# Kernel optimization log

Measured on AMD Instinct MI355X. Metric: run time of the kernel, lower is better.

The kernel has to match this reference:

```python
import jax, jax.numpy as jnp
import numpy as np
import math

B, L, D, H = 32, 512, 4096, 32
HD = D // H  # head_dim = 128


def setup_inputs() -> dict:
    key = jax.random.key(0)
    ks = jax.random.split(key, 9)
    s = 1.0 / math.sqrt(D)
    return {
        "x": jax.random.normal(ks[0], (B, L, D), jnp.float32),
        "Wq": jax.random.normal(ks[1], (D, D), jnp.float32) * s,
        "bq": jax.random.normal(ks[2], (D,), jnp.float32) * s,
        "Wk": jax.random.normal(ks[3], (D, D), jnp.float32) * s,
        "bk": jax.random.normal(ks[4], (D,), jnp.float32) * s,
        "Wv": jax.random.normal(ks[5], (D, D), jnp.float32) * s,
        "bv": jax.random.normal(ks[6], (D,), jnp.float32) * s,
        "Wo": jax.random.normal(ks[7], (D, D), jnp.float32) * s,
        "bo": jax.random.normal(ks[8], (D,), jnp.float32) * s,
    }


def reference(x, Wq, bq, Wk, bk, Wv, bv, Wo, bo):
    b, l, d = x.shape
    h, hd = H, HD
    # torch Linear: y = x @ W.T + b
    q = (x @ Wq.T + bq).reshape(b, l, h, hd).transpose(0, 2, 1, 3)  # [b,h,l,hd]
    k = (x @ Wk.T + bk).reshape(b, l, h, hd).transpose(0, 2, 1, 3)
    v = (x @ Wv.T + bv).reshape(b, l, h, hd).transpose(0, 2, 1, 3)
    scores = jnp.einsum("bhqd,bhkd->bhqk", q, k) / math.sqrt(hd)  # [b,h,L,L]
    # causal mask (upper triangle, diagonal=1, excluded)
    causal = jnp.tril(jnp.ones((l, l), bool))
    scores = jnp.where(causal, scores, -jnp.inf)
    att = jax.nn.softmax(scores, axis=-1)
    out = jnp.einsum("bhqk,bhkd->bhqd", att, v)  # [b,h,L,hd]
    out = out.transpose(0, 2, 1, 3).reshape(b, l, d)
    return out @ Wo.T + bo
```

## Files before the change

kernel.cpp:

```cpp
#include <hip/hip_runtime.h>
#include <cstdint>
#include <cstddef>

typedef __bf16 bf16_t;
typedef __bf16 bf16x8 __attribute__((ext_vector_type(8)));
typedef float f32x4 __attribute__((ext_vector_type(4)));

#define LOG2E 1.4426950408889634f

__device__ __forceinline__ void async16(const void* g, void* l) {
  __builtin_amdgcn_global_load_lds(
      (__attribute__((address_space(1))) unsigned int*)g,
      (__attribute__((address_space(3))) unsigned int*)l, 16, 0, 0);
}

__global__ void mha_cast_bf16(const float* __restrict__ s, bf16_t* __restrict__ d) {
  size_t i = (size_t)blockIdx.x * 256 + threadIdx.x;
  const float4* s4 = (const float4*)s;
  float4 a = s4[2 * i], b = s4[2 * i + 1];
  union { bf16_t h[8]; uint4 v; } u;
  u.h[0] = (bf16_t)a.x; u.h[1] = (bf16_t)a.y; u.h[2] = (bf16_t)a.z; u.h[3] = (bf16_t)a.w;
  u.h[4] = (bf16_t)b.x; u.h[5] = (bf16_t)b.y; u.h[6] = (bf16_t)b.z; u.h[7] = (bf16_t)b.w;
  ((uint4*)d)[i] = u.v;
}

__global__ void mha_cast_cat3(const float* __restrict__ s0, const float* __restrict__ s1,
                              const float* __restrict__ s2, bf16_t* __restrict__ d) {
  size_t i = (size_t)blockIdx.x * 256 + threadIdx.x;
  size_t e = i * 8;
  int r = (int)(e >> 24);
  const float* s = (r == 0) ? s0 : ((r == 1) ? s1 : s2);
  size_t off = e & 0xFFFFFFull;
  const float4* s4 = (const float4*)(s + off);
  float4 a = s4[0], b = s4[1];
  union { bf16_t h[8]; uint4 v; } u;
  u.h[0] = (bf16_t)a.x; u.h[1] = (bf16_t)a.y; u.h[2] = (bf16_t)a.z; u.h[3] = (bf16_t)a.w;
  u.h[4] = (bf16_t)b.x; u.h[5] = (bf16_t)b.y; u.h[6] = (bf16_t)b.z; u.h[7] = (bf16_t)b.w;
  ((uint4*)d)[i] = u.v;
}

template <int OUTF32>
__global__ __launch_bounds__(256, 2) void mha_gemm_bt(
    const bf16_t* __restrict__ A, const bf16_t* __restrict__ B,
    const float* __restrict__ b0, const float* __restrict__ b1,
    const float* __restrict__ b2, void* __restrict__ Cp,
    int N, int K, int tilesN) {
  __shared__ bf16_t As[128 * 32];
  __shared__ bf16_t Bs[128 * 32];
  const int tid = threadIdx.x;
  const int lane = tid & 63, w = tid >> 6;
  const int quad = lane >> 4, l16 = lane & 15;
  const int bm = blockIdx.x / tilesN, bn = blockIdx.x % tilesN;
  const int row0 = bm * 128, col0 = bn * 128;
  const int wm = (w >> 1) * 64, wn = (w & 1) * 64;

  f32x4 acc[4][4] = {};

  const int c0 = tid, c1 = 256 + tid;
  const int k80 = c0 >> 7, m0 = c0 & 127;
  const int k81 = c1 >> 7, m1 = c1 & 127;
  const bf16_t* gA0 = A + (size_t)(row0 + m0) * K + k80 * 8;
  const bf16_t* gA1 = A + (size_t)(row0 + m1) * K + k81 * 8;
  const bf16_t* gB0 = B + (size_t)(col0 + m0) * K + k80 * 8;
  const bf16_t* gB1 = B + (size_t)(col0 + m1) * K + k81 * 8;
  bf16_t* lA0 = As + (w * 64) * 8;
  bf16_t* lA1 = As + (256 + w * 64) * 8;
  bf16_t* lB0 = Bs + (w * 64) * 8;
  bf16_t* lB1 = Bs + (256 + w * 64) * 8;

  for (int k0 = 0; k0 < K; k0 += 32) {
    async16(gA0, lA0); async16(gA1, lA1);
    async16(gB0, lB0); async16(gB1, lB1);
    gA0 += 32; gA1 += 32; gB0 += 32; gB1 += 32;
    __syncthreads();
    bf16x8 af[4], bfr[4];
#pragma unroll
    for (int t = 0; t < 4; ++t)
      af[t] = *(const bf16x8*)(As + (quad * 128 + wm + 16 * t + l16) * 8);
#pragma unroll
    for (int u = 0; u < 4; ++u)
      bfr[u] = *(const bf16x8*)(Bs + (quad * 128 + wn + 16 * u + l16) * 8);
#pragma unroll
    for (int t = 0; t < 4; ++t)
#pragma unroll
      for (int u = 0; u < 4; ++u)
        acc[t][u] = __builtin_amdgcn_mfma_f32_16x16x32_bf16(af[t], bfr[u], acc[t][u], 0, 0, 0);
    __syncthreads();
  }

#pragma unroll
  for (int u = 0; u < 4; ++u) {
    int col = col0 + wn + 16 * u + l16;
    int sel = col >> 12;
    const float* bb = (sel == 0) ? b0 : ((sel == 1) ? b1 : b2);
    float bias = bb[col & 4095];
#pragma unroll
    for (int t = 0; t < 4; ++t) {
#pragma unroll
      for (int r = 0; r < 4; ++r) {
        int row = row0 + wm + 16 * t + quad * 4 + r;
        float val = acc[t][u][r] + bias;
        if (OUTF32)
          ((float*)Cp)[(size_t)row * N + col] = val;
        else
          ((bf16_t*)Cp)[(size_t)row * N + col] = (bf16_t)val;
      }
    }
  }
}

__global__ __launch_bounds__(256, 2) void mha_attn(const bf16_t* __restrict__ qkv,
                                                   bf16_t* __restrict__ out) {
  __shared__ bf16_t Ks[64 * 128];
  __shared__ bf16_t R2[128 * 128];
  const int tid = threadIdx.x;
  const int lane = tid & 63, w = tid >> 6;
  const int quad = lane >> 4, l16 = lane & 15;
  const int qt = blockIdx.x & 3;
  const int h = (blockIdx.x >> 2) & 31;
  const int b = blockIdx.x >> 7;
  const float scale = 0.08838834764831845f;
  const size_t rs = 12288;

  const bf16_t* baseQ = qkv + (size_t)(b * 512 + qt * 128) * rs + h * 128;
#pragma unroll
  for (int i = 0; i < 8; ++i) {
    int c = i * 256 + tid;
    int hd8 = c >> 7, m = c & 127;
    async16(baseQ + (size_t)m * rs + hd8 * 8, R2 + (i * 256 + w * 64) * 8);
  }
  __syncthreads();
  bf16x8 qf[2][4];
#pragma unroll
  for (int t = 0; t < 2; ++t)
#pragma unroll
    for (int kk = 0; kk < 4; ++kk)
      qf[t][kk] = *(const bf16x8*)(R2 + ((kk * 4 + quad) * 128 + w * 32 + 16 * t + l16) * 8);

  f32x4 O[2][8] = {};
  float mrow[2][4], lrow[2][4];
#pragma unroll
  for (int t = 0; t < 2; ++t)
#pragma unroll
    for (int r = 0; r < 4; ++r) { mrow[t][r] = -1e30f; lrow[t][r] = 0.f; }

  bf16_t* Vts = R2;
  bf16_t* Ps = R2 + 8192 + w * 2048;

  const int ktEnd = 2 * qt + 1;
  for (int kt = 0; kt <= ktEnd; ++kt) {
    __syncthreads();
    const bf16_t* baseK = qkv + (size_t)(b * 512 + kt * 64) * rs + 4096 + h * 128;
#pragma unroll
    for (int i = 0; i < 4; ++i) {
      int c = i * 256 + tid;
      int hd8 = c >> 6, key = c & 63;
      async16(baseK + (size_t)key * rs + hd8 * 8, Ks + (i * 256 + w * 64) * 8);
    }
    const bf16_t* baseV = qkv + (size_t)(b * 512 + kt * 64) * rs + 8192 + h * 128;
#pragma unroll
    for (int j = 0; j < 4; ++j) {
      int idx = j * 256 + tid;
      int d8 = idx & 15, key = idx >> 4;
      bf16x8 vv = *(const bf16x8*)(baseV + (size_t)key * rs + d8 * 8);
#pragma unroll
      for (int e = 0; e < 8; ++e) {
        int ee = (e + d8) & 7;
        int d = d8 * 8 + ee;
        Vts[((key >> 3) * 128 + d) * 8 + (key & 7)] = vv[ee];
      }
    }
    __syncthreads();

    f32x4 S[2][4] = {};
#pragma unroll
    for (int kk = 0; kk < 4; ++kk) {
      bf16x8 kf[4];
#pragma unroll
      for (int u = 0; u < 4; ++u)
        kf[u] = *(const bf16x8*)(Ks + ((kk * 4 + quad) * 64 + 16 * u + l16) * 8);
#pragma unroll
      for (int t = 0; t < 2; ++t)
#pragma unroll
        for (int u = 0; u < 4; ++u)
          S[t][u] = __builtin_amdgcn_mfma_f32_16x16x32_bf16(qf[t][kk], kf[u], S[t][u], 0, 0, 0);
    }

    const bool maskTile = (kt >= 2 * qt);
#pragma unroll
    for (int t = 0; t < 2; ++t) {
      int qbase = qt * 128 + w * 32 + 16 * t + quad * 4;
#pragma unroll
      for (int u = 0; u < 4; ++u) {
        int key = kt * 64 + 16 * u + l16;
#pragma unroll
        for (int r = 0; r < 4; ++r) {
          float v = S[t][u][r] * scale;
          if (maskTile && key > qbase + r) v = -1e30f;
          S[t][u][r] = v;
        }
      }
    }

#pragma unroll
    for (int t = 0; t < 2; ++t) {
#pragma unroll
      for (int r = 0; r < 4; ++r) {
        float mx = fmaxf(fmaxf(S[t][0][r], S[t][1][r]), fmaxf(S[t][2][r], S[t][3][r]));
        mx = fmaxf(mx, __shfl_xor(mx, 1));
        mx = fmaxf(mx, __shfl_xor(mx, 2));
        mx = fmaxf(mx, __shfl_xor(mx, 4));
        mx = fmaxf(mx, __shfl_xor(mx, 8));
        float mnew = fmaxf(mrow[t][r], mx);
        float alpha = exp2f((mrow[t][r] - mnew) * LOG2E);
        mrow[t][r] = mnew;
        float psum = 0.f;
#pragma unroll
        for (int u = 0; u < 4; ++u) {
          float p = exp2f((S[t][u][r] - mnew) * LOG2E);
          S[t][u][r] = p;
          psum += p;
        }
        psum += __shfl_xor(psum, 1);
        psum += __shfl_xor(psum, 2);
        psum += __shfl_xor(psum, 4);
        psum += __shfl_xor(psum, 8);
        lrow[t][r] = lrow[t][r] * alpha + psum;
#pragma unroll
        for (int u = 0; u < 8; ++u) O[t][u][r] *= alpha;
      }
    }

#pragma unroll
    for (int t = 0; t < 2; ++t)
#pragma unroll
      for (int u = 0; u < 4; ++u) {
        int key = 16 * u + l16;
#pragma unroll
        for (int rr = 0; rr < 4; ++rr) {
          int r = (rr + quad) & 3;
          Ps[((key >> 3) * 32 + 16 * t + quad * 4 + r) * 8 + (key & 7)] = (bf16_t)S[t][u][r];
        }
      }

#pragma unroll
    for (int kk = 0; kk < 2; ++kk) {
      bf16x8 pf[2], vf[8];
#pragma unroll
      for (int t = 0; t < 2; ++t)
        pf[t] = *(const bf16x8*)(Ps + ((kk * 4 + quad) * 32 + 16 * t + l16) * 8);
#pragma unroll
      for (int u = 0; u < 8; ++u)
        vf[u] = *(const bf16x8*)(Vts + ((kk * 4 + quad) * 128 + 16 * u + l16) * 8);
#pragma unroll
      for (int t = 0; t < 2; ++t)
#pragma unroll
        for (int u = 0; u < 8; ++u)
          O[t][u] = __builtin_amdgcn_mfma_f32_16x16x32_bf16(pf[t], vf[u], O[t][u], 0, 0, 0);
    }
  }

  bf16_t* outBase = out + (size_t)(b * 512 + qt * 128) * 4096 + h * 128;
#pragma unroll
  for (int t = 0; t < 2; ++t)
#pragma unroll
    for (int u = 0; u < 8; ++u) {
      int d = 16 * u + l16;
#pragma unroll
      for (int r = 0; r < 4; ++r) {
        int q = w * 32 + 16 * t + quad * 4 + r;
        float val = O[t][u][r] / lrow[t][r];
        outBase[(size_t)q * 4096 + d] = (bf16_t)val;
      }
    }
}

extern "C" void kernel_launch(void* const* d_in, const int* in_sizes, int n_in,
                              void* d_out, int out_size, void* d_ws, size_t ws_size,
                              hipStream_t stream) {
  const float* x  = (const float*)d_in[0];
  const float* Wq = (const float*)d_in[1];
  const float* bq = (const float*)d_in[2];
  const float* Wk = (const float*)d_in[3];
  const float* bk = (const float*)d_in[4];
  const float* Wv = (const float*)d_in[5];
  const float* bv = (const float*)d_in[6];
  const float* Wo = (const float*)d_in[7];
  const float* bo = (const float*)d_in[8];

  char* ws = (char*)d_ws;
  bf16_t* xb   = (bf16_t*)ws;
  bf16_t* wqkv = (bf16_t*)(ws + 134217728ull);
  bf16_t* wob  = (bf16_t*)(ws + 134217728ull + 100663296ull);
  bf16_t* qkvb = (bf16_t*)(ws + 134217728ull + 100663296ull + 33554432ull);

  mha_cast_bf16<<<32768, 256, 0, stream>>>(x, xb);
  mha_cast_cat3<<<24576, 256, 0, stream>>>(Wq, Wk, Wv, wqkv);
  mha_cast_bf16<<<8192, 256, 0, stream>>>(Wo, wob);

  mha_gemm_bt<0><<<12288, 256, 0, stream>>>(xb, wqkv, bq, bk, bv, qkvb, 12288, 4096, 96);

  mha_attn<<<4096, 256, 0, stream>>>(qkvb, xb);

  mha_gemm_bt<1><<<4096, 256, 0, stream>>>(xb, wob, bo, bo, bo, d_out, 4096, 4096, 32);
}
```

Baseline: 5.897 ms.

## Rewrite GEMM with 256x256 tiles, double-buffered async LDS and grid swizzle

Replaces the 128x128, single-buffered GEMM with a 512-thread 256x256 tile that double-buffers K=64 slices in 128KB of LDS using async global-to-LDS loads. Loads for the next-but-one tile are issued between the two MFMA halves, so memory traffic overlaps compute and the per-iteration sync shrinks to a waitcnt plus barrier. A blockIdx swizzle groups workgroups to improve L2 reuse. The cost is higher register pressure (128 accumulator floats per thread) and large LDS use, which limits occupancy to about one workgroup per CU.

```diff
diff --git a/kernel.cpp b/kernel.cpp
--- a/kernel.cpp
+++ b/kernel.cpp
@@ -39,67 +39,107 @@
   ((uint4*)d)[i] = u.v;
 }
 
+__device__ __forceinline__ void stage8(const bf16_t* ga, const bf16_t* gb,
+                                       bf16_t* la, bf16_t* lb) {
+  async16(ga,      la);
+  async16(ga + 16, la + 4096);
+  async16(ga + 32, la + 8192);
+  async16(ga + 48, la + 12288);
+  async16(gb,      lb);
+  async16(gb + 16, lb + 4096);
+  async16(gb + 32, lb + 8192);
+  async16(gb + 48, lb + 12288);
+}
+
 template <int OUTF32>
-__global__ __launch_bounds__(256, 2) void mha_gemm_bt(
+__global__ __launch_bounds__(512, 2) void mha_gemm_bt(
     const bf16_t* __restrict__ A, const bf16_t* __restrict__ B,
     const float* __restrict__ b0, const float* __restrict__ b1,
     const float* __restrict__ b2, void* __restrict__ Cp,
     int N, int K, int tilesN) {
-  __shared__ bf16_t As[128 * 32];
-  __shared__ bf16_t Bs[128 * 32];
+  __shared__ bf16_t LDS[65536];
   const int tid = threadIdx.x;
   const int lane = tid & 63, w = tid >> 6;
   const int quad = lane >> 4, l16 = lane & 15;
-  const int bm = blockIdx.x / tilesN, bn = blockIdx.x % tilesN;
-  const int row0 = bm * 128, col0 = bn * 128;
-  const int wm = (w >> 1) * 64, wn = (w & 1) * 64;
-
-  f32x4 acc[4][4] = {};
-
-  const int c0 = tid, c1 = 256 + tid;
-  const int k80 = c0 >> 7, m0 = c0 & 127;
-  const int k81 = c1 >> 7, m1 = c1 & 127;
-  const bf16_t* gA0 = A + (size_t)(row0 + m0) * K + k80 * 8;
-  const bf16_t* gA1 = A + (size_t)(row0 + m1) * K + k81 * 8;
-  const bf16_t* gB0 = B + (size_t)(col0 + m0) * K + k80 * 8;
-  const bf16_t* gB1 = B + (size_t)(col0 + m1) * K + k81 * 8;
-  bf16_t* lA0 = As + (w * 64) * 8;
-  bf16_t* lA1 = As + (256 + w * 64) * 8;
-  bf16_t* lB0 = Bs + (w * 64) * 8;
-  bf16_t* lB1 = Bs + (256 + w * 64) * 8;
-
-  for (int k0 = 0; k0 < K; k0 += 32) {
-    async16(gA0, lA0); async16(gA1, lA1);
-    async16(gB0, lB0); async16(gB1, lB1);
-    gA0 += 32; gA1 += 32; gB0 += 32; gB1 += 32;
-    __syncthreads();
-    bf16x8 af[4], bfr[4];
-#pragma unroll
-    for (int t = 0; t < 4; ++t)
-      af[t] = *(const bf16x8*)(As + (quad * 128 + wm + 16 * t + l16) * 8);
-#pragma unroll
-    for (int u = 0; u < 4; ++u)
-      bfr[u] = *(const bf16x8*)(Bs + (quad * 128 + wn + 16 * u + l16) * 8);
-#pragma unroll
-    for (int t = 0; t < 4; ++t)
+  const int wr = w >> 2, wc = w & 3;
+
+  int wgid = blockIdx.x;
+  const int nwg = gridDim.x;
+  if ((nwg & 7) == 0) wgid = (wgid & 7) * (nwg >> 3) + (wgid >> 3);
+  const int bm = wgid / tilesN, bn = wgid % tilesN;
+  const int row0 = bm * 256, col0 = bn * 256;
+
+  const int ms = tid & 255, khi = tid >> 8;
+  const bf16_t* gA = A + (size_t)(row0 + ms) * K + khi * 8;
+  const bf16_t* gB = B + (size_t)(col0 + ms) * K + khi * 8;
+  bf16_t* la = LDS + w * 512;
+  bf16_t* lb = LDS + 16384 + w * 512;
+
+  const bf16_t* ar = LDS + (quad * 256 + wr * 128 + l16) * 8;
+  const bf16_t* br = LDS + (16384) + (quad * 256 + wc * 64 + l16) * 8;
+
+  f32x4 acc[8][4] = {};
+
+  const int NT = K >> 6;
+  stage8(gA, gB, la, lb);
+  stage8(gA + 64, gB + 64, la + 32768, lb + 32768);
+  asm volatile("s_waitcnt vmcnt(8)" ::: "memory");
+  __builtin_amdgcn_s_barrier();
+
+  for (int t = 0; t < NT; ++t) {
+    const int boff = (t & 1) << 15;
+    const bf16_t* aptr = ar + boff;
+    const bf16_t* bptr = br + boff;
+
+    bf16x8 fa0[8], fb0[4];
+#pragma unroll
+    for (int i = 0; i < 8; ++i) fa0[i] = *(const bf16x8*)(aptr + i * 128);
+#pragma unroll
+    for (int u = 0; u < 4; ++u) fb0[u] = *(const bf16x8*)(bptr + u * 128);
+#pragma unroll
+    for (int i = 0; i < 8; ++i)
 #pragma unroll
       for (int u = 0; u < 4; ++u)
-        acc[t][u] = __builtin_amdgcn_mfma_f32_16x16x32_bf16(af[t], bfr[u], acc[t][u], 0, 0, 0);
-    __syncthreads();
+        acc[i][u] = __builtin_amdgcn_mfma_f32_16x16x32_bf16(fa0[i], fb0[u], acc[i][u], 0, 0, 0);
+
+    bf16x8 fa1[8], fb1[4];
+#pragma unroll
+    for (int i = 0; i < 8; ++i) fa1[i] = *(const bf16x8*)(aptr + 8192 + i * 128);
+#pragma unroll
+    for (int u = 0; u < 4; ++u) fb1[u] = *(const bf16x8*)(bptr + 8192 + u * 128);
+
+    asm volatile("s_waitcnt lgkmcnt(0)" ::: "memory");
+    __builtin_amdgcn_s_barrier();
+
+    if (t + 2 < NT)
+      stage8(gA + (size_t)(t + 2) * 64, gB + (size_t)(t + 2) * 64, la + boff, lb + boff);
+
+#pragma unroll
+    for (int i = 0; i < 8; ++i)
+#pragma unroll
+      for (int u = 0; u < 4; ++u)
+        acc[i][u] = __builtin_amdgcn_mfma_f32_16x16x32_bf16(fa1[i], fb1[u], acc[i][u], 0, 0, 0);
+
+    __builtin_amdgcn_sched_barrier(0);
+    if (t + 1 < NT) {
+      if (t + 2 < NT) asm volatile("s_waitcnt vmcnt(8)" ::: "memory");
+      else            asm volatile("s_waitcnt vmcnt(0)" ::: "memory");
+      __builtin_amdgcn_s_barrier();
+    }
   }
 
 #pragma unroll
   for (int u = 0; u < 4; ++u) {
-    int col = col0 + wn + 16 * u + l16;
+    int col = col0 + wc * 64 + 16 * u + l16;
     int sel = col >> 12;
     const float* bb = (sel == 0) ? b0 : ((sel == 1) ? b1 : b2);
     float bias = bb[col & 4095];
 #pragma unroll
-    for (int t = 0; t < 4; ++t) {
+    for (int i = 0; i < 8; ++i) {
 #pragma unroll
       for (int r = 0; r < 4; ++r) {
-        int row = row0 + wm + 16 * t + quad * 4 + r;
-        float val = acc[t][u][r] + bias;
+        int row = row0 + wr * 128 + 16 * i + quad * 4 + r;
+        float val = acc[i][u][r] + bias;
         if (OUTF32)
           ((float*)Cp)[(size_t)row * N + col] = val;
         else
@@ -298,9 +338,9 @@
   mha_cast_cat3<<<24576, 256, 0, stream>>>(Wq, Wk, Wv, wqkv);
   mha_cast_bf16<<<8192, 256, 0, stream>>>(Wo, wob);
 
-  mha_gemm_bt<0><<<12288, 256, 0, stream>>>(xb, wqkv, bq, bk, bv, qkvb, 12288, 4096, 96);
+  mha_gemm_bt<0><<<3072, 512, 0, stream>>>(xb, wqkv, bq, bk, bv, qkvb, 12288, 4096, 48);
 
   mha_attn<<<4096, 256, 0, stream>>>(qkvb, xb);
 
-  mha_gemm_bt<1><<<4096, 256, 0, stream>>>(xb, wob, bo, bo, bo, d_out, 4096, 4096, 32);
-}
+  mha_gemm_bt<1><<<1024, 512, 0, stream>>>(xb, wob, bo, bo, bo, d_out, 4096, 4096, 16);
+}
```

After: 4.854 ms. 1.21x faster.
